# Kernel tuning notes

Measured on AMD Instinct MI355X. Metric: run time of the kernel, lower is better.

Reference implementation:

```python
import jax, jax.numpy as jnp
import numpy as np

VOCAB, EMBED, HIDDEN = 32000, 512, 1024
B, T = 2, 2048
LN_EPS = 1e-5


def setup_inputs() -> dict:
    key = jax.random.key(0)
    ks = jax.random.split(key, 12)

    def xavier(k, fan_in, fan_out):
        lim = float(np.sqrt(6.0 / (fan_in + fan_out)))
        return jax.random.uniform(k, (fan_in, fan_out), jnp.float32, -lim, lim)

    return {
        "tokens": jax.random.randint(ks[0], (B, T), 0, VOCAB),
        "E": xavier(ks[1], VOCAB, EMBED),                    # embedding table
        "Wc": xavier(ks[2], EMBED, HIDDEN),                  # fc_current (stored [in,out])
        "bc": jnp.full((HIDDEN,), 0.01, jnp.float32),
        "Wh": xavier(ks[3], EMBED, HIDDEN),                  # fc_context
        "bh": jnp.full((HIDDEN,), 0.01, jnp.float32),
        "Wm": xavier(ks[4], 2 * HIDDEN, HIDDEN),             # fc_merge
        "bm": jnp.full((HIDDEN,), 0.01, jnp.float32),
        "Wo": xavier(ks[5], HIDDEN, VOCAB),                  # fc_out
        "bo": jnp.full((VOCAB,), 0.01, jnp.float32),
        "ln_w": jnp.ones((HIDDEN,), jnp.float32),
        "ln_b": jnp.zeros((HIDDEN,), jnp.float32),
    }


def reference(tokens, E, Wc, bc, Wh, bh, Wm, bm, Wo, bo, ln_w, ln_b):
    emb = E[tokens]  # [B, T, D]
    # history mean at step t = mean(emb[:, :t]); at t==0 the module uses current embed
    csum = jnp.cumsum(emb, axis=1)
    counts = jnp.arange(1, T, dtype=emb.dtype)[None, :, None]
    hist_mean = jnp.concatenate([emb[:, :1], csum[:, :-1] / counts], axis=1)  # [B,T,D]

    cur_enc = jax.nn.relu(jnp.einsum("btd,dh->bth", emb, Wc) + bc)
    hist_enc = jax.nn.relu(jnp.einsum("btd,dh->bth", hist_mean, Wh) + bh)
    merged = jnp.concatenate([cur_enc, hist_enc], axis=-1)  # [B,T,2H]
    merged = jax.nn.relu(jnp.einsum("btk,kh->bth", merged, Wm) + bm)

    mu = jnp.mean(merged, axis=-1, keepdims=True)
    var = jnp.mean(jnp.square(merged - mu), axis=-1, keepdims=True)
    normed = (merged - mu) * jax.lax.rsqrt(var + LN_EPS) * ln_w + ln_b

    logits = (jnp.einsum("bth,hv->btv", normed, Wo) + bo) / 10.0  # [B,T,V]
    return logits
```

## Files before the change

kernel.cpp:

```cpp
#include <hip/hip_runtime.h>
#include <hip/hip_bf16.h>
#include <stdint.h>
#include <stdio.h>

#define T_SEQ  2048
#define BATCH  2
#define NROWS  4096
#define EMBED  512
#define HIDDEN 1024
#define VOCAB  32000
#define NCHUNK 128
#define CHLEN  16

typedef __bf16 bf16x8 __attribute__((ext_vector_type(8)));
typedef float  f32x4  __attribute__((ext_vector_type(4)));

__device__ __forceinline__ float b2f(unsigned short h) {
  union { unsigned int u; float f; } v; v.u = ((unsigned int)h) << 16; return v.f;
}
__device__ __forceinline__ unsigned short f2b(float f) {
  union { float f; unsigned int u; } v; v.f = f;
  unsigned int u = v.u;
  u += 0x7fffu + ((u >> 16) & 1u);
  return (unsigned short)(u >> 16);
}

__device__ __forceinline__ void async16(unsigned short* lds, const unsigned short* g) {
  __builtin_amdgcn_global_load_lds(
      (const __attribute__((address_space(1))) void*)g,
      (__attribute__((address_space(3))) void*)lds, 16, 0, 0);
}

__global__ __launch_bounds__(512) void prep_kernel(
    const int* __restrict__ tokens, const float* __restrict__ E,
    unsigned short* __restrict__ emb, float* __restrict__ csum,
    const float* __restrict__ Wc, const float* __restrict__ Wh,
    const float* __restrict__ Wm, const float* __restrict__ Wo,
    unsigned short* __restrict__ WcT, unsigned short* __restrict__ WhT,
    unsigned short* __restrict__ WmT, unsigned short* __restrict__ WoT) {
  const int id = blockIdx.x;

  if (id >= 8768) {
    const int bc = id - 8768;
    const int d  = threadIdx.x;
    __shared__ int tok[CHLEN];
    if (d < CHLEN) tok[d] = tokens[bc * CHLEN + d];
    __syncthreads();
    float s = 0.f;
    unsigned short* eo = emb + ((size_t)bc * CHLEN) * EMBED + d;
    #pragma unroll 4
    for (int i = 0; i < CHLEN; ++i) {
      const float v = E[(size_t)tok[i] * EMBED + d];
      const unsigned short h = f2b(v);
      eo[(size_t)i * EMBED] = h;
      s += b2f(h);
    }
    csum[(size_t)bc * EMBED + d] = s;
    return;
  }

  const float* in; unsigned short* out; int R, C, t;
  if (id < 128)      { in = Wc; out = WcT; R = 512;  C = 1024;  t = id; }
  else if (id < 256) { in = Wh; out = WhT; R = 512;  C = 1024;  t = id - 128; }
  else if (id < 768) { in = Wm; out = WmT; R = 2048; C = 1024;  t = id - 256; }
  else               { in = Wo; out = WoT; R = 1024; C = 32000; t = id - 768; }
  const int tilesX = C >> 6;
  const int r0 = (t / tilesX) << 6, c0 = (t % tilesX) << 6;

  __shared__ float tile[64][65];
  const int tid = threadIdx.x;
  #pragma unroll
  for (int p = 0; p < 2; ++p) {
    const int u = tid + p * 512;
    const int row = u >> 4, cq = (u & 15) << 2;
    const float4 v = *(const float4*)&in[(size_t)(r0 + row) * C + c0 + cq];
    tile[row][cq + 0] = v.x; tile[row][cq + 1] = v.y;
    tile[row][cq + 2] = v.z; tile[row][cq + 3] = v.w;
  }
  __syncthreads();
  #pragma unroll
  for (int p = 0; p < 2; ++p) {
    const int u = tid + p * 512;
    const int oc = u >> 4, org = (u & 15) << 2;
    ushort4 o;
    o.x = f2b(tile[org + 0][oc]); o.y = f2b(tile[org + 1][oc]);
    o.z = f2b(tile[org + 2][oc]); o.w = f2b(tile[org + 3][oc]);
    *(ushort4*)&out[(size_t)(c0 + oc) * R + r0 + org] = o;
  }
}

__global__ void scan_excl_kernel(float* __restrict__ csum) {
  const int b  = blockIdx.x;
  const int d0 = blockIdx.y << 7;
  const int t  = threadIdx.x;
  __shared__ float s[NCHUNK][128];
  for (int c = 0; c < NCHUNK; ++c)
    s[c][t] = csum[((size_t)b * NCHUNK + c) * EMBED + d0 + t];
  float run = 0.f;
  for (int c = 0; c < NCHUNK; ++c) {
    const float v = s[c][t];
    csum[((size_t)b * NCHUNK + c) * EMBED + d0 + t] = run;
    run += v;
  }
}

__global__ void scan_emit_kernel(const unsigned short* __restrict__ emb,
                                 const float* __restrict__ csum,
                                 unsigned short* __restrict__ hist) {
  const int bc = blockIdx.x;
  const int c  = bc & (NCHUNK - 1);
  const int d  = threadIdx.x;
  const unsigned short* e = emb  + ((size_t)bc * CHLEN) * EMBED + d;
  unsigned short*       h = hist + ((size_t)bc * CHLEN) * EMBED + d;
  float sum = csum[(size_t)bc * EMBED + d];
  #pragma unroll 8
  for (int i = 0; i < CHLEN; ++i) {
    const int t = c * CHLEN + i;
    h[(size_t)i * EMBED] = (t == 0) ? e[0] : f2b(sum / (float)t);
    sum += b2f(e[(size_t)i * EMBED]);
  }
}

#define BM 128
#define BN 128
#define BK 32

template<int MODE>
__global__ __launch_bounds__(256) void gemm_bt_kernel(
    const unsigned short* __restrict__ A,
    const unsigned short* __restrict__ BT,
    const float* __restrict__ bias,
    void* __restrict__ out, int M, int N, int K, int ldOut, int colOff,
    const unsigned short* __restrict__ A2,
    const unsigned short* __restrict__ BT2,
    const float* __restrict__ bias2, int colOff2) {
  __shared__ unsigned short As[2][BM * BK];
  __shared__ unsigned short Bs[2][BN * BK];

  const unsigned short* Ap = A;
  const unsigned short* Bp = BT;
  const float*          bp = bias;
  int                   co = colOff;
  if (blockIdx.z) { Ap = A2; Bp = BT2; bp = bias2; co = colOff2; }

  int wg = blockIdx.x;
  {
    const int nwg = gridDim.x;
    const int xcd = wg & 7, loc = wg >> 3;
    const int q = nwg >> 3, r = nwg & 7;
    wg = (xcd < r ? xcd * (q + 1) : r * (q + 1) + (xcd - r) * q) + loc;
  }
  const int nmb = M / BM;
  const int mb  = wg % nmb;
  const int nb  = wg / nmb;
  const int m0  = mb * BM;
  const int n0  = nb * BN;

  const int tid  = threadIdx.x;
  const int wave = tid >> 6;
  const int lane = tid & 63;
  const int wm = (wave & 1) * 64;
  const int wn = (wave >> 1) * 64;

  const int srow = (wave << 5) + (lane >> 2);
  const int scol = (lane & 3) << 3;
  const unsigned short* aSrc = Ap + (size_t)(m0 + srow) * K + scol;
  const unsigned short* bSrc = Bp + (size_t)(n0 + srow) * K + scol;
  const int ldsOff = (wave << 5) * BK;

  f32x4 acc[4][4];
  #pragma unroll
  for (int i = 0; i < 4; ++i)
    #pragma unroll
    for (int j = 0; j < 4; ++j)
      acc[i][j] = (f32x4){0.f, 0.f, 0.f, 0.f};

  const int q = lane >> 4;
  const int r = lane & 15;

  auto stageT = [&](int buf) {
    async16(&As[buf][ldsOff],           aSrc);
    async16(&As[buf][ldsOff + 16 * BK], aSrc + 16 * (size_t)K);
    async16(&Bs[buf][ldsOff],           bSrc);
    async16(&Bs[buf][ldsOff + 16 * BK], bSrc + 16 * (size_t)K);
    aSrc += BK; bSrc += BK;
  };

  const int nt = K / BK;
  stageT(0);
  __syncthreads();

  for (int t = 0; t < nt; ++t) {
    const int c = t & 1;
    if (t + 1 < nt) stageT(1 - c);

    bf16x8 af[4], bfr[4];
    #pragma unroll
    for (int mi = 0; mi < 4; ++mi)
      af[mi] = *(const bf16x8*)&As[c][(wm + mi * 16 + r) * BK + (q << 3)];
    #pragma unroll
    for (int ni = 0; ni < 4; ++ni)
      bfr[ni] = *(const bf16x8*)&Bs[c][(wn + ni * 16 + r) * BK + (q << 3)];
    #pragma unroll
    for (int mi = 0; mi < 4; ++mi)
      #pragma unroll
      for (int ni = 0; ni < 4; ++ni)
        acc[mi][ni] = __builtin_amdgcn_mfma_f32_16x16x32_bf16(
            af[mi], bfr[ni], acc[mi][ni], 0, 0, 0);

    __syncthreads();
  }

  #pragma unroll
  for (int ni = 0; ni < 4; ++ni) {
    const int col = n0 + wn + ni * 16 + r;
    const float bv = bp[col];
    #pragma unroll
    for (int mi = 0; mi < 4; ++mi) {
      #pragma unroll
      for (int e = 0; e < 4; ++e) {
        const int row = m0 + wm + mi * 16 + (q << 2) + e;
        float v = fmaxf(acc[mi][ni][e] + bv, 0.f);
        const size_t idx = (size_t)row * ldOut + co + col;
        if (MODE == 0) ((unsigned short*)out)[idx] = f2b(v);
        else           ((float*)out)[idx] = v;
      }
    }
  }
}


#define BAR() do {                            \
    asm volatile("" ::: "memory");            \
    __builtin_amdgcn_sched_barrier(0);        \
    __builtin_amdgcn_s_barrier();             \
    __builtin_amdgcn_sched_barrier(0);        \
    asm volatile("" ::: "memory");            \
  } while (0)

__global__ __launch_bounds__(512, 2) void gemm256_out_kernel(
    const unsigned short* __restrict__ A,
    const unsigned short* __restrict__ BT,
    const float* __restrict__ bias,
    float* __restrict__ out, int M, int N, int K, int ldOut) {
  __shared__ unsigned short lds[2][2][2][8192];

  int wg = blockIdx.x;
  {
    const int nwg = gridDim.x;
    const int xcd = wg & 7, loc = wg >> 3;
    const int q8 = nwg >> 3, r8 = nwg & 7;
    wg = (xcd < r8 ? xcd * (q8 + 1) : r8 * (q8 + 1) + (xcd - r8) * q8) + loc;
  }
  const int nmb = M >> 8;
  const int mb = wg % nmb, nb = wg / nmb;
  const int m0 = mb << 8, n0 = nb << 8;

  const int tid  = threadIdx.x;
  const int wave = tid >> 6, lane = tid & 63;
  const int wr = wave >> 2, wc = wave & 3;
  const int q = lane >> 4, r = lane & 15, rr = lane & 7;

  const int srow = (wave << 4) + (lane >> 3);
  const int scol = ((lane & 7) ^ (lane >> 3)) << 3;
  const unsigned short* aB = A  + (size_t)(m0 + srow) * K + scol;
  const unsigned short* bB = BT + (size_t)(n0 + srow) * K + scol;

  const int NTt = K >> 6;

  auto stage = [&](int matB, int h, int tb, int kt) {
    unsigned short* d = &lds[tb][matB][h][wave << 10];
    const unsigned short* s =
        (matB ? bB : aB) + (size_t)h * 128 * K + ((size_t)kt << 6);
    async16(d, s);
    async16(d + 512, s + ((size_t)K << 3));
  };

  auto ldA = [&](int tb, int mi, int ks) {
    return *(const bf16x8*)&lds[tb][0][wr]
        [(mi * 16 + r) * 64 + ((((ks << 2) | q) ^ rr) << 3)];
  };
  auto ldB = [&](int tb, int ni, int ks) {
    return *(const bf16x8*)&lds[tb][1][wc >> 1]
        [(((wc & 1) << 6) + ni * 16 + r) * 64 + ((((ks << 2) | q) ^ rr) << 3)];
  };

  f32x4 acc[8][4];
  #pragma unroll
  for (int i = 0; i < 8; ++i)
    #pragma unroll
    for (int j = 0; j < 4; ++j)
      acc[i][j] = (f32x4){0.f, 0.f, 0.f, 0.f};

  bf16x8 afr[8][2], bfr[2][2];

  stage(0, 0, 0, 0); stage(0, 1, 0, 0); stage(1, 0, 0, 0); stage(1, 1, 0, 0);
  if (NTt > 1) {
    stage(0, 0, 1, 1); stage(0, 1, 1, 1); stage(1, 0, 1, 1);
    asm volatile("s_waitcnt vmcnt(6)" ::: "memory");
  } else {
    asm volatile("s_waitcnt vmcnt(0)" ::: "memory");
  }
  BAR();

#define TILE(U, BU) do {                                                       \
    const int u_ = (U);                                                        \
                            \
    _Pragma("unroll")                                                          \
    for (int mi = 0; mi < 4; ++mi) {                                           \
      afr[mi][0] = ldA(BU, mi, 0); afr[mi][1] = ldA(BU, mi, 1);                \
    }                                                                          \
    _Pragma("unroll")                                                          \
    for (int nj = 0; nj < 2; ++nj) {                                           \
      bfr[nj][0] = ldB(BU, nj, 0); bfr[nj][1] = ldB(BU, nj, 1);                \
    }                                                                          \
    if (u_ + 1 < NTt) stage(1, 1, 1 - (BU), u_ + 1);                           \
    __builtin_amdgcn_s_setprio(1);                                             \
    _Pragma("unroll")                                                          \
    for (int mi = 0; mi < 4; ++mi)                                             \
      _Pragma("unroll")                                                        \
      for (int nj = 0; nj < 2; ++nj) {                                         \
        acc[mi][nj] = __builtin_amdgcn_mfma_f32_16x16x32_bf16(                 \
            afr[mi][0], bfr[nj][0], acc[mi][nj], 0, 0, 0);                     \
        acc[mi][nj] = __builtin_amdgcn_mfma_f32_16x16x32_bf16(                 \
            afr[mi][1], bfr[nj][1], acc[mi][nj], 0, 0, 0);                     \
      }                                                                        \
    __builtin_amdgcn_s_setprio(0);                                             \
    BAR();                                                                     \
                                 \
    _Pragma("unroll")                                                          \
    for (int mi = 4; mi < 8; ++mi) {                                           \
      afr[mi][0] = ldA(BU, mi, 0); afr[mi][1] = ldA(BU, mi, 1);                \
    }                                                                          \
    __builtin_amdgcn_s_setprio(1);                                             \
    _Pragma("unroll")                                                          \
    for (int mi = 4; mi < 8; ++mi)                                             \
      _Pragma("unroll")                                                        \
      for (int nj = 0; nj < 2; ++nj) {                                         \
        acc[mi][nj] = __builtin_amdgcn_mfma_f32_16x16x32_bf16(                 \
            afr[mi][0], bfr[nj][0], acc[mi][nj], 0, 0, 0);                     \
        acc[mi][nj] = __builtin_amdgcn_mfma_f32_16x16x32_bf16(                 \
            afr[mi][1], bfr[nj][1], acc[mi][nj], 0, 0, 0);                     \
      }                                                                        \
    __builtin_amdgcn_s_setprio(0);                                             \
    BAR();                                                                     \
                            \
    _Pragma("unroll")                                                          \
    for (int nj = 0; nj < 2; ++nj) {                                           \
      bfr[nj][0] = ldB(BU, 2 + nj, 0); bfr[nj][1] = ldB(BU, 2 + nj, 1);        \
    }                                                                          \
    if (u_ + 2 < NTt) stage(0, 0, BU, u_ + 2);                                 \
    __builtin_amdgcn_s_setprio(1);                                             \
    _Pragma("unroll")                                                          \
    for (int mi = 0; mi < 4; ++mi)                                             \
      _Pragma("unroll")                                                        \
      for (int nj = 0; nj < 2; ++nj) {                                         \
        acc[mi][2 + nj] = __builtin_amdgcn_mfma_f32_16x16x32_bf16(             \
            afr[mi][0], bfr[nj][0], acc[mi][2 + nj], 0, 0, 0);                 \
        acc[mi][2 + nj] = __builtin_amdgcn_mfma_f32_16x16x32_bf16(             \
            afr[mi][1], bfr[nj][1], acc[mi][2 + nj], 0, 0, 0);                 \
      }                                                                        \
    __builtin_amdgcn_s_setprio(0);                                             \
    BAR();                                                                     \
                   \
    if (u_ + 2 < NTt) { stage(0, 1, BU, u_ + 2); stage(1, 0, BU, u_ + 2); }    \
    __builtin_amdgcn_s_setprio(1);                                             \
    _Pragma("unroll")                                                          \
    for (int mi = 4; mi < 8; ++mi)                                             \
      _Pragma("unroll")                                                        \
      for (int nj = 0; nj < 2; ++nj) {                                         \
        acc[mi][2 + nj] = __builtin_amdgcn_mfma_f32_16x16x32_bf16(             \
            afr[mi][0], bfr[nj][0], acc[mi][2 + nj], 0, 0, 0);                 \
        acc[mi][2 + nj] = __builtin_amdgcn_mfma_f32_16x16x32_bf16(             \
            afr[mi][1], bfr[nj][1], acc[mi][2 + nj], 0, 0, 0);                 \
      }                                                                        \
    __builtin_amdgcn_s_setprio(0);                                             \
    if (u_ + 2 < NTt) asm volatile("s_waitcnt vmcnt(6)" ::: "memory");         \
    else              asm volatile("s_waitcnt vmcnt(0)" ::: "memory");         \
    BAR();                                                                     \
  } while (0)

  for (int u = 0; u < NTt; u += 2) {
    TILE(u, 0);
    TILE(u + 1, 1);
  }
#undef TILE

  float* scratch = (float*)&lds[0][0][0][0];
  #pragma unroll
  for (int p = 0; p < 2; ++p) {
    if (wr == p) {
      #pragma unroll
      for (int ni = 0; ni < 4; ++ni) {
        const int col = (wc << 6) + ni * 16 + r;
        const float bv = bias[n0 + col];
        #pragma unroll
        for (int mi = 0; mi < 8; ++mi) {
          #pragma unroll
          for (int e = 0; e < 4; ++e) {
            const int row = mi * 16 + (q << 2) + e;
            const int cs  = col ^ (((row >> 2) & 1) << 4);
            scratch[row * 256 + cs] = (acc[mi][ni][e] + bv) * 0.1f;
          }
        }
      }
    }
    __syncthreads();
    #pragma unroll
    for (int rowi = 0; rowi < 16; ++rowi) {
      const int row = (wave << 4) + rowi;
      const int cb  = (lane << 2) ^ (((row >> 2) & 1) << 4);
      const f32x4 v4 = *(const f32x4*)&scratch[row * 256 + cb];
      __builtin_nontemporal_store(
          v4, (f32x4*)&out[(size_t)(m0 + (p << 7) + row) * ldOut + n0 + (lane << 2)]);
    }
    __syncthreads();
  }
}

__global__ void ln_kernel(const float* __restrict__ merged,
                          const float* __restrict__ lnw,
                          const float* __restrict__ lnb,
                          unsigned short* __restrict__ normed) {
  const int row = blockIdx.x;
  const float4 v = ((const float4*)(merged + (size_t)row * HIDDEN))[threadIdx.x];
  float s  = v.x + v.y + v.z + v.w;
  float ss = v.x * v.x + v.y * v.y + v.z * v.z + v.w * v.w;
  #pragma unroll
  for (int off = 32; off > 0; off >>= 1) {
    s  += __shfl_down(s, off, 64);
    ss += __shfl_down(ss, off, 64);
  }
  __shared__ float red[8];
  const int wvi = threadIdx.x >> 6;
  if ((threadIdx.x & 63) == 0) { red[wvi] = s; red[4 + wvi] = ss; }
  __syncthreads();
  s  = red[0] + red[1] + red[2] + red[3];
  ss = red[4] + red[5] + red[6] + red[7];
  const float mu  = s * (1.0f / HIDDEN);
  const float var = ss * (1.0f / HIDDEN) - mu * mu;
  const float rs  = rsqrtf(var + 1e-5f);
  const float4 w4 = ((const float4*)lnw)[threadIdx.x];
  const float4 b4 = ((const float4*)lnb)[threadIdx.x];
  ushort4 o;
  o.x = f2b((v.x - mu) * rs * w4.x + b4.x);
  o.y = f2b((v.y - mu) * rs * w4.y + b4.y);
  o.z = f2b((v.z - mu) * rs * w4.z + b4.z);
  o.w = f2b((v.w - mu) * rs * w4.w + b4.w);
  ((ushort4*)(normed + (size_t)row * HIDDEN))[threadIdx.x] = o;
}

extern "C" void kernel_launch(void* const* d_in, const int* in_sizes, int n_in,
                              void* d_out, int out_size, void* d_ws, size_t ws_size,
                              hipStream_t stream) {
  const int*   tokens = (const int*)d_in[0];
  const float* E      = (const float*)d_in[1];
  const float* Wc     = (const float*)d_in[2];
  const float* bc     = (const float*)d_in[3];
  const float* Wh     = (const float*)d_in[4];
  const float* bh     = (const float*)d_in[5];
  const float* Wm     = (const float*)d_in[6];
  const float* bm     = (const float*)d_in[7];
  const float* Wo     = (const float*)d_in[8];
  const float* bo     = (const float*)d_in[9];
  const float* lnw    = (const float*)d_in[10];
  const float* lnb    = (const float*)d_in[11];

  char* p = (char*)d_ws;
  unsigned short* WcT  = (unsigned short*)p; p += (size_t)HIDDEN * EMBED * 2;
  unsigned short* WhT  = (unsigned short*)p; p += (size_t)HIDDEN * EMBED * 2;
  unsigned short* WmT  = (unsigned short*)p; p += (size_t)HIDDEN * (2 * HIDDEN) * 2;
  unsigned short* WoT  = (unsigned short*)p; p += (size_t)VOCAB * HIDDEN * 2;
  unsigned short* emb  = (unsigned short*)p; p += (size_t)NROWS * EMBED * 2;
  unsigned short* hist = (unsigned short*)p; p += (size_t)NROWS * EMBED * 2;
  unsigned short* cat  = (unsigned short*)p; p += (size_t)NROWS * (2 * HIDDEN) * 2;
  float*          mrg  = (float*)p;          p += (size_t)NROWS * HIDDEN * 4;
  unsigned short* nrm  = (unsigned short*)p; p += (size_t)NROWS * HIDDEN * 2;
  float*          csum = (float*)p;          p += (size_t)BATCH * NCHUNK * EMBED * 4;
  if ((size_t)(p - (char*)d_ws) > ws_size)
    fprintf(stderr, "WS TOO SMALL: need %zu have %zu\n", (size_t)(p - (char*)d_ws), ws_size);

  prep_kernel<<<8768 + 256, 512, 0, stream>>>(
      tokens, E, emb, csum, Wc, Wh, Wm, Wo, WcT, WhT, WmT, WoT);
  scan_excl_kernel<<<dim3(BATCH, EMBED / 128), 128, 0, stream>>>(csum);
  scan_emit_kernel<<<BATCH * NCHUNK, EMBED, 0, stream>>>(emb, csum, hist);

  const int nwgEnc = (NROWS / BM) * (HIDDEN / BN);

  gemm_bt_kernel<0><<<dim3(nwgEnc, 1, 2), 256, 0, stream>>>(
      emb, WcT, bc, cat, NROWS, HIDDEN, EMBED, 2 * HIDDEN, 0,
      hist, WhT, bh, HIDDEN);
  gemm_bt_kernel<1><<<dim3(nwgEnc, 1, 1), 256, 0, stream>>>(
      cat, WmT, bm, mrg, NROWS, HIDDEN, 2 * HIDDEN, HIDDEN, 0,
      nullptr, nullptr, nullptr, 0);
  ln_kernel<<<NROWS, 256, 0, stream>>>(mrg, lnw, lnb, nrm);

  const int nwgOut = (NROWS / 256) * (VOCAB / 256);
  gemm256_out_kernel<<<dim3(nwgOut), 512, 0, stream>>>(
      nrm, WoT, bo, (float*)d_out, NROWS, VOCAB, HIDDEN, VOCAB);
}
```

Baseline: 939.9 us.

## Shrink output GEMM tile to 128x256 with K-step 32 for higher occupancy

Reworks the vocabulary projection GEMM from a 256x256 tile with K-step 64 to a 128x256 tile with K-step 32. LDS use and accumulator registers per block are cut, so launch bounds ask for 4 blocks per CU and the grid doubles. The staging, swizzle and epilogue are rewritten to match. The goal is more waves in flight to hide latency and better balance across CUs, at the cost of less A/B reuse per block, more barriers per unit of K, and more global traffic for the weight matrix.

```diff
diff --git a/kernel.cpp b/kernel.cpp
--- a/kernel.cpp
+++ b/kernel.cpp
@@ -238,12 +238,14 @@
     asm volatile("" ::: "memory");            \
   } while (0)
 
-__global__ __launch_bounds__(512, 2) void gemm256_out_kernel(
+struct OutLds { unsigned short A[4096]; unsigned short B[8192]; };
+
+__global__ __launch_bounds__(512, 4) void gemm_out_kernel(
     const unsigned short* __restrict__ A,
     const unsigned short* __restrict__ BT,
     const float* __restrict__ bias,
     float* __restrict__ out, int M, int N, int K, int ldOut) {
-  __shared__ unsigned short lds[2][2][2][8192];
+  __shared__ OutLds lds[2];
 
   int wg = blockIdx.x;
   {
@@ -252,167 +254,124 @@
     const int q8 = nwg >> 3, r8 = nwg & 7;
     wg = (xcd < r8 ? xcd * (q8 + 1) : r8 * (q8 + 1) + (xcd - r8) * q8) + loc;
   }
-  const int nmb = M >> 8;
+  const int nmb = M >> 7;
   const int mb = wg % nmb, nb = wg / nmb;
-  const int m0 = mb << 8, n0 = nb << 8;
+  const int m0 = mb << 7, n0 = nb << 8;
 
   const int tid  = threadIdx.x;
   const int wave = tid >> 6, lane = tid & 63;
   const int wr = wave >> 2, wc = wave & 3;
-  const int q = lane >> 4, r = lane & 15, rr = lane & 7;
-
-  const int srow = (wave << 4) + (lane >> 3);
-  const int scol = ((lane & 7) ^ (lane >> 3)) << 3;
+  const int q = lane >> 4, r = lane & 15;
+  const int sw = (r >> 1) & 3;
+
+  const int srow = (wave << 4) + (lane >> 2);
+  const int scol = ((lane & 3) ^ ((lane >> 3) & 3)) << 3;
   const unsigned short* aB = A  + (size_t)(m0 + srow) * K + scol;
   const unsigned short* bB = BT + (size_t)(n0 + srow) * K + scol;
 
-  const int NTt = K >> 6;
-
-  auto stage = [&](int matB, int h, int tb, int kt) {
-    unsigned short* d = &lds[tb][matB][h][wave << 10];
-    const unsigned short* s =
-        (matB ? bB : aB) + (size_t)h * 128 * K + ((size_t)kt << 6);
-    async16(d, s);
-    async16(d + 512, s + ((size_t)K << 3));
+  const int NTt = K >> 5;
+
+  auto stageA = [&](int tb, int kt) {
+    async16(&lds[tb].A[wave << 9], aB + ((size_t)kt << 5));
   };
-
-  auto ldA = [&](int tb, int mi, int ks) {
-    return *(const bf16x8*)&lds[tb][0][wr]
-        [(mi * 16 + r) * 64 + ((((ks << 2) | q) ^ rr) << 3)];
+  auto stageB = [&](int tb, int kt) {
+    async16(&lds[tb].B[wave << 9],          bB + ((size_t)kt << 5));
+    async16(&lds[tb].B[4096 + (wave << 9)], bB + (size_t)128 * K + ((size_t)kt << 5));
   };
-  auto ldB = [&](int tb, int ni, int ks) {
-    return *(const bf16x8*)&lds[tb][1][wc >> 1]
-        [(((wc & 1) << 6) + ni * 16 + r) * 64 + ((((ks << 2) | q) ^ rr) << 3)];
+
+  auto ldA = [&](int tb, int mi) {
+    const int row = (wr << 6) + mi * 16 + r;
+    return *(const bf16x8*)&lds[tb].A[(row << 5) + ((q ^ sw) << 3)];
   };
-
-  f32x4 acc[8][4];
-  #pragma unroll
-  for (int i = 0; i < 8; ++i)
+  auto ldB = [&](int tb, int nj) {
+    const int row = (wc << 6) + nj * 16 + r;
+    return *(const bf16x8*)&lds[tb].B[(row << 5) + ((q ^ sw) << 3)];
+  };
+
+  f32x4 acc[4][4];
+  #pragma unroll
+  for (int i = 0; i < 4; ++i)
     #pragma unroll
     for (int j = 0; j < 4; ++j)
       acc[i][j] = (f32x4){0.f, 0.f, 0.f, 0.f};
 
-  bf16x8 afr[8][2], bfr[2][2];
-
-  stage(0, 0, 0, 0); stage(0, 1, 0, 0); stage(1, 0, 0, 0); stage(1, 1, 0, 0);
+  bf16x8 afr[4], bfr[2];
+
+  stageA(0, 0); stageB(0, 0);
   if (NTt > 1) {
-    stage(0, 0, 1, 1); stage(0, 1, 1, 1); stage(1, 0, 1, 1);
-    asm volatile("s_waitcnt vmcnt(6)" ::: "memory");
+    stageA(1, 1);
+    asm volatile("s_waitcnt vmcnt(1)" ::: "memory");
   } else {
     asm volatile("s_waitcnt vmcnt(0)" ::: "memory");
   }
   BAR();
 
-#define TILE(U, BU) do {                                                       \
+#define OTILE(U, BU) do {                                                      \
     const int u_ = (U);                                                        \
-                            \
+          \
     _Pragma("unroll")                                                          \
-    for (int mi = 0; mi < 4; ++mi) {                                           \
-      afr[mi][0] = ldA(BU, mi, 0); afr[mi][1] = ldA(BU, mi, 1);                \
-    }                                                                          \
-    _Pragma("unroll")                                                          \
-    for (int nj = 0; nj < 2; ++nj) {                                           \
-      bfr[nj][0] = ldB(BU, nj, 0); bfr[nj][1] = ldB(BU, nj, 1);                \
-    }                                                                          \
-    if (u_ + 1 < NTt) stage(1, 1, 1 - (BU), u_ + 1);                           \
+    for (int mi = 0; mi < 4; ++mi) afr[mi] = ldA(BU, mi);                      \
+    bfr[0] = ldB(BU, 0); bfr[1] = ldB(BU, 1);                                  \
+    if (u_ + 1 < NTt) stageB(1 - (BU), u_ + 1);                                \
     __builtin_amdgcn_s_setprio(1);                                             \
     _Pragma("unroll")                                                          \
     for (int mi = 0; mi < 4; ++mi)                                             \
       _Pragma("unroll")                                                        \
-      for (int nj = 0; nj < 2; ++nj) {                                         \
+      for (int nj = 0; nj < 2; ++nj)                                           \
         acc[mi][nj] = __builtin_amdgcn_mfma_f32_16x16x32_bf16(                 \
-            afr[mi][0], bfr[nj][0], acc[mi][nj], 0, 0, 0);                     \
-        acc[mi][nj] = __builtin_amdgcn_mfma_f32_16x16x32_bf16(                 \
-            afr[mi][1], bfr[nj][1], acc[mi][nj], 0, 0, 0);                     \
-      }                                                                        \
+            afr[mi], bfr[nj], acc[mi][nj], 0, 0, 0);                           \
     __builtin_amdgcn_s_setprio(0);                                             \
-    BAR();                                                                     \
-                                 \
-    _Pragma("unroll")                                                          \
-    for (int mi = 4; mi < 8; ++mi) {                                           \
-      afr[mi][0] = ldA(BU, mi, 0); afr[mi][1] = ldA(BU, mi, 1);                \
-    }                                                                          \
-    __builtin_amdgcn_s_setprio(1);                                             \
-    _Pragma("unroll")                                                          \
-    for (int mi = 4; mi < 8; ++mi)                                             \
-      _Pragma("unroll")                                                        \
-      for (int nj = 0; nj < 2; ++nj) {                                         \
-        acc[mi][nj] = __builtin_amdgcn_mfma_f32_16x16x32_bf16(                 \
-            afr[mi][0], bfr[nj][0], acc[mi][nj], 0, 0, 0);                     \
-        acc[mi][nj] = __builtin_amdgcn_mfma_f32_16x16x32_bf16(                 \
-            afr[mi][1], bfr[nj][1], acc[mi][nj], 0, 0, 0);                     \
-      }                                                                        \
-    __builtin_amdgcn_s_setprio(0);                                             \
-    BAR();                                                                     \
-                            \
-    _Pragma("unroll")                                                          \
-    for (int nj = 0; nj < 2; ++nj) {                                           \
-      bfr[nj][0] = ldB(BU, 2 + nj, 0); bfr[nj][1] = ldB(BU, 2 + nj, 1);        \
-    }                                                                          \
-    if (u_ + 2 < NTt) stage(0, 0, BU, u_ + 2);                                 \
+    BAR();                                   \
+           \
+    bfr[0] = ldB(BU, 2); bfr[1] = ldB(BU, 3);                                  \
+    if (u_ + 2 < NTt) stageA(BU, u_ + 2);                                      \
     __builtin_amdgcn_s_setprio(1);                                             \
     _Pragma("unroll")                                                          \
     for (int mi = 0; mi < 4; ++mi)                                             \
       _Pragma("unroll")                                                        \
-      for (int nj = 0; nj < 2; ++nj) {                                         \
+      for (int nj = 0; nj < 2; ++nj)                                           \
         acc[mi][2 + nj] = __builtin_amdgcn_mfma_f32_16x16x32_bf16(             \
-            afr[mi][0], bfr[nj][0], acc[mi][2 + nj], 0, 0, 0);                 \
-        acc[mi][2 + nj] = __builtin_amdgcn_mfma_f32_16x16x32_bf16(             \
-            afr[mi][1], bfr[nj][1], acc[mi][2 + nj], 0, 0, 0);                 \
-      }                                                                        \
+            afr[mi], bfr[nj], acc[mi][2 + nj], 0, 0, 0);                       \
     __builtin_amdgcn_s_setprio(0);                                             \
-    BAR();                                                                     \
-                   \
-    if (u_ + 2 < NTt) { stage(0, 1, BU, u_ + 2); stage(1, 0, BU, u_ + 2); }    \
-    __builtin_amdgcn_s_setprio(1);                                             \
-    _Pragma("unroll")                                                          \
-    for (int mi = 4; mi < 8; ++mi)                                             \
-      _Pragma("unroll")                                                        \
-      for (int nj = 0; nj < 2; ++nj) {                                         \
-        acc[mi][2 + nj] = __builtin_amdgcn_mfma_f32_16x16x32_bf16(             \
-            afr[mi][0], bfr[nj][0], acc[mi][2 + nj], 0, 0, 0);                 \
-        acc[mi][2 + nj] = __builtin_amdgcn_mfma_f32_16x16x32_bf16(             \
-            afr[mi][1], bfr[nj][1], acc[mi][2 + nj], 0, 0, 0);                 \
-      }                                                                        \
-    __builtin_amdgcn_s_setprio(0);                                             \
-    if (u_ + 2 < NTt) asm volatile("s_waitcnt vmcnt(6)" ::: "memory");         \
+    if (u_ + 2 < NTt) asm volatile("s_waitcnt vmcnt(1)" ::: "memory");         \
     else              asm volatile("s_waitcnt vmcnt(0)" ::: "memory");         \
-    BAR();                                                                     \
+    BAR();                                  \
   } while (0)
 
   for (int u = 0; u < NTt; u += 2) {
-    TILE(u, 0);
-    TILE(u + 1, 1);
-  }
-#undef TILE
-
-  float* scratch = (float*)&lds[0][0][0][0];
-  #pragma unroll
-  for (int p = 0; p < 2; ++p) {
-    if (wr == p) {
+    OTILE(u, 0);
+    OTILE(u + 1, 1);
+  }
+#undef OTILE
+
+  float* scratch = (float*)&lds[0];
+  #pragma unroll
+  for (int p = 0; p < 4; ++p) {
+    if (wr == (p >> 1)) {
+      const int mibase = (p & 1) << 1;
       #pragma unroll
       for (int ni = 0; ni < 4; ++ni) {
         const int col = (wc << 6) + ni * 16 + r;
         const float bv = bias[n0 + col];
         #pragma unroll
-        for (int mi = 0; mi < 8; ++mi) {
+        for (int mi2 = 0; mi2 < 2; ++mi2) {
           #pragma unroll
           for (int e = 0; e < 4; ++e) {
-            const int row = mi * 16 + (q << 2) + e;
+            const int row = mi2 * 16 + (q << 2) + e;
             const int cs  = col ^ (((row >> 2) & 1) << 4);
-            scratch[row * 256 + cs] = (acc[mi][ni][e] + bv) * 0.1f;
+            scratch[row * 256 + cs] = (acc[mibase + mi2][ni][e] + bv) * 0.1f;
           }
         }
       }
     }
     __syncthreads();
     #pragma unroll
-    for (int rowi = 0; rowi < 16; ++rowi) {
-      const int row = (wave << 4) + rowi;
+    for (int i = 0; i < 4; ++i) {
+      const int row = (wave << 2) + i;
       const int cb  = (lane << 2) ^ (((row >> 2) & 1) << 4);
       const f32x4 v4 = *(const f32x4*)&scratch[row * 256 + cb];
       __builtin_nontemporal_store(
-          v4, (f32x4*)&out[(size_t)(m0 + (p << 7) + row) * ldOut + n0 + (lane << 2)]);
+          v4, (f32x4*)&out[(size_t)(m0 + (p << 5) + row) * ldOut + n0 + (lane << 2)]);
     }
     __syncthreads();
   }
@@ -495,7 +454,7 @@
       nullptr, nullptr, nullptr, 0);
   ln_kernel<<<NROWS, 256, 0, stream>>>(mrg, lnw, lnb, nrm);
 
-  const int nwgOut = (NROWS / 256) * (VOCAB / 256);
-  gemm256_out_kernel<<<dim3(nwgOut), 512, 0, stream>>>(
+  const int nwgOut = (NROWS / 128) * (VOCAB / 256);
+  gemm_out_kernel<<<dim3(nwgOut), 512, 0, stream>>>(
       nrm, WoT, bo, (float*)d_out, NROWS, VOCAB, HIDDEN, VOCAB);
 }
```

Measured after the change: 953.5 us. Within noise of the previous version (+1.4%).
